# Kernel tuning notes

Measured on AMD Instinct MI355X. Metric: run time of the kernel, lower is better.

## Reference

```python
import jax, jax.numpy as jnp
import numpy as np

B, S, DIM = 4, 2048, 64
NUM_CODES = 65536
KCODES = 8


def setup_inputs() -> dict:
    key = jax.random.key(0)
    k1, k2 = jax.random.split(key)
    x = jax.random.normal(k1, (B, S, DIM), dtype=jnp.float32)
    codebook = jax.random.normal(k2, (NUM_CODES, DIM), dtype=jnp.float32)
    return {"x": x, "codebook": codebook}


def reference(x, codebook):
    """EuclideanSnapFunction.forward, keep_k_codes path with no disabled codes.

    logits = -cdist(x, codebook, p=2); topk(kcodes); embedding gather; mean.
    sqrt is monotonic, so top-k on negative *squared* distance yields identical
    indices (and identical outputs) while avoiding the sqrt.
    """
    x2 = jnp.sum(x * x, axis=-1, keepdims=True)          # [B,S,1]
    c2 = jnp.sum(codebook * codebook, axis=-1)           # [N]
    xc = jnp.einsum("bsd,nd->bsn", x, codebook)          # [B,S,N]
    neg_d2 = 2.0 * xc - x2 - c2                           # = -squared dist
    _, codebook_ids = jax.lax.top_k(neg_d2, KCODES)      # [B,S,K]
    codes = codebook[codebook_ids]                        # [B,S,K,D] gather
    outputs = codes.sum(axis=-2) / KCODES                 # [B,S,D]
    return outputs, codebook_ids
```

## Files before the change

kernel.cpp:

```cpp
#include <hip/hip_runtime.h>
#include <float.h>

#define DIM     64
#define NCODES  65536
#define KC      8
#define NQ      8192
#define KROW    80
#define CS      64
#define CHUNK   (NCODES/CS)
#define NITER   (CHUNK/32)
#define NVIEW   128
#define CAP     7
#define DELTA   0.75f
#define MAXSUR  512
#define CSA     32
#define CHUNKA  512
#define NITERA  (CHUNKA/32)
#define NVIEWA  64

typedef __bf16 bf16x8 __attribute__((ext_vector_type(8)));
typedef float  f32x16 __attribute__((ext_vector_type(16)));
typedef unsigned short u16x8 __attribute__((ext_vector_type(8)));

static __device__ __forceinline__ unsigned short f2bf(float f) {
    unsigned u = __float_as_uint(f);
    u += 0x7FFFu + ((u >> 16) & 1u);
    return (unsigned short)(u >> 16);
}

#define RJ(j) (((j) & 3) + 8 * ((j) >> 2))

__global__ __launch_bounds__(256) void k_conv_cb(const float* __restrict__ cb,
                                                 unsigned short* __restrict__ cbb) {
    int n = blockIdx.x * 256 + threadIdx.x;
    const float4* src = (const float4*)(cb + (size_t)n * DIM);
    unsigned short* dst = cbb + (size_t)n * KROW;
    float s = 0.f;
#pragma unroll
    for (int c = 0; c < 8; ++c) {
        float4 f0 = src[2 * c], f1 = src[2 * c + 1];
        s = fmaf(f0.x, f0.x, s); s = fmaf(f0.y, f0.y, s);
        s = fmaf(f0.z, f0.z, s); s = fmaf(f0.w, f0.w, s);
        s = fmaf(f1.x, f1.x, s); s = fmaf(f1.y, f1.y, s);
        s = fmaf(f1.z, f1.z, s); s = fmaf(f1.w, f1.w, s);
        u16x8 o;
        o[0] = f2bf(2.f * f0.x); o[1] = f2bf(2.f * f0.y);
        o[2] = f2bf(2.f * f0.z); o[3] = f2bf(2.f * f0.w);
        o[4] = f2bf(2.f * f1.x); o[5] = f2bf(2.f * f1.y);
        o[6] = f2bf(2.f * f1.z); o[7] = f2bf(2.f * f1.w);
        *(u16x8*)(dst + c * 8) = o;
    }
    unsigned short hi = f2bf(s);
    float hif = __uint_as_float(((unsigned)hi) << 16);
    unsigned short lo = f2bf(s - hif);
    u16x8 p = { (unsigned short)(hi ^ 0x8000u), (unsigned short)(lo ^ 0x8000u),
                0, 0, 0, 0, 0, 0 };
    *(u16x8*)(dst + 64) = p;
    u16x8 z = {0, 0, 0, 0, 0, 0, 0, 0};
    *(u16x8*)(dst + 72) = z;
}

__global__ __launch_bounds__(256) void k_conv_x(const float* __restrict__ x,
                                                unsigned short* __restrict__ xb) {
    int n = blockIdx.x * 256 + threadIdx.x;
    const float4* src = (const float4*)(x + (size_t)n * DIM);
    unsigned short* dst = xb + (size_t)n * KROW;
#pragma unroll
    for (int c = 0; c < 8; ++c) {
        float4 f0 = src[2 * c], f1 = src[2 * c + 1];
        u16x8 o;
        o[0] = f2bf(f0.x); o[1] = f2bf(f0.y); o[2] = f2bf(f0.z); o[3] = f2bf(f0.w);
        o[4] = f2bf(f1.x); o[5] = f2bf(f1.y); o[6] = f2bf(f1.z); o[7] = f2bf(f1.w);
        *(u16x8*)(dst + c * 8) = o;
    }
    u16x8 p = {0x3F80u, 0x3F80u, 0, 0, 0, 0, 0, 0};
    *(u16x8*)(dst + 64) = p;
    u16x8 z = {0, 0, 0, 0, 0, 0, 0, 0};
    *(u16x8*)(dst + 72) = z;
}

__device__ __forceinline__ float tmax16(const f32x16& a) {
    const float m0 = fmaxf(fmaxf(a[0],  a[1]),  a[2]);
    const float m1 = fmaxf(fmaxf(a[3],  a[4]),  a[5]);
    const float m2 = fmaxf(fmaxf(a[6],  a[7]),  a[8]);
    const float m3 = fmaxf(fmaxf(a[9],  a[10]), a[11]);
    const float m4 = fmaxf(fmaxf(a[12], a[13]), a[14]);
    const float n0 = fmaxf(fmaxf(m0, m1), m2);
    const float n1 = fmaxf(fmaxf(m3, m4), a[15]);
    return fmaxf(n0, n1);
}

__global__ __launch_bounds__(256, 4) void k_scanA(const unsigned short* __restrict__ cbb_,
                                                  const unsigned short* __restrict__ xb_,
                                                  float* __restrict__ top1) {
    const __bf16* cbv = (const __bf16*)cbb_;
    const __bf16* xbv = (const __bf16*)xb_;
    const int tid = threadIdx.x, lane = tid & 63, wv = tid >> 6;
    const int laneh = lane >> 5;
    const int qg = blockIdx.x >> 5;
    const int cs = blockIdx.x & 31;
    const int qA = qg * 256 + wv * 64 + (lane & 31);
    const int qB = qA + 32;
    const int cbase = cs * CHUNKA;
    const int view = cs * 2 + laneh;

    bf16x8 bfrA[5], bfrB[5];
    {
        const __bf16* bp = xbv + (size_t)qA * KROW + laneh * 8;
#pragma unroll
        for (int s = 0; s < 5; ++s) bfrA[s] = *(const bf16x8*)(bp + s * 16);
        bp += (size_t)32 * KROW;
#pragma unroll
        for (int s = 0; s < 5; ++s) bfrB[s] = *(const bf16x8*)(bp + s * 16);
    }

    float t1a = -FLT_MAX, t1b = -FLT_MAX;

    const __bf16* ap = cbv + (size_t)(cbase + (lane & 31)) * KROW + laneh * 8;
    bf16x8 fA[5], fB[5];
#pragma unroll
    for (int s = 0; s < 5; ++s) fA[s] = *(const bf16x8*)(ap + s * 16);
#pragma unroll
    for (int s = 0; s < 5; ++s) fB[s] = *(const bf16x8*)(ap + 32 * KROW + s * 16);
    ap += 64 * KROW;

    for (int it = 0; it < NITERA; it += 2) {
        {
            f32x16 acc = {0,0,0,0, 0,0,0,0, 0,0,0,0, 0,0,0,0};
#pragma unroll
            for (int s = 0; s < 5; ++s)
                acc = __builtin_amdgcn_mfma_f32_32x32x16_bf16(fA[s], bfrA[s], acc, 0, 0, 0);
            t1a = fmaxf(t1a, tmax16(acc));
            f32x16 acc2 = {0,0,0,0, 0,0,0,0, 0,0,0,0, 0,0,0,0};
#pragma unroll
            for (int s = 0; s < 5; ++s)
                acc2 = __builtin_amdgcn_mfma_f32_32x32x16_bf16(fA[s], bfrB[s], acc2, 0, 0, 0);
#pragma unroll
            for (int s = 0; s < 5; ++s) fA[s] = *(const bf16x8*)(ap + s * 16);
            t1b = fmaxf(t1b, tmax16(acc2));
        }
        {
            f32x16 acc = {0,0,0,0, 0,0,0,0, 0,0,0,0, 0,0,0,0};
#pragma unroll
            for (int s = 0; s < 5; ++s)
                acc = __builtin_amdgcn_mfma_f32_32x32x16_bf16(fB[s], bfrA[s], acc, 0, 0, 0);
            t1a = fmaxf(t1a, tmax16(acc));
            f32x16 acc2 = {0,0,0,0, 0,0,0,0, 0,0,0,0, 0,0,0,0};
#pragma unroll
            for (int s = 0; s < 5; ++s)
                acc2 = __builtin_amdgcn_mfma_f32_32x32x16_bf16(fB[s], bfrB[s], acc2, 0, 0, 0);
#pragma unroll
            for (int s = 0; s < 5; ++s) fB[s] = *(const bf16x8*)(ap + 32 * KROW + s * 16);
            t1b = fmaxf(t1b, tmax16(acc2));
        }
        ap += 64 * KROW;
    }

    top1[(size_t)qA * NVIEWA + view] = t1a;
    top1[(size_t)qB * NVIEWA + view] = t1b;
}

__global__ __launch_bounds__(256) void k_thresh(const float* __restrict__ top1,
                                                float* __restrict__ thrm) {
    const int lane = threadIdx.x & 63;
    const int q = blockIdx.x * 4 + (threadIdx.x >> 6);
    float v = top1[(size_t)q * NVIEWA + lane];
    float mx = -FLT_MAX;
#pragma unroll
    for (int r = 0; r < 8; ++r) {
        mx = v;
#pragma unroll
        for (int off = 32; off; off >>= 1) mx = fmaxf(mx, __shfl_xor(mx, off, 64));
        if (v == mx) v = -FLT_MAX;
    }
    if (lane == 0) thrm[q] = mx - DELTA;
}

__global__ __launch_bounds__(256, 4) void k_collect(const unsigned short* __restrict__ cbb_,
                                                    const unsigned short* __restrict__ xb_,
                                                    const float* __restrict__ thrm,
                                                    unsigned short* __restrict__ cand,
                                                    unsigned char* __restrict__ cnt) {
    const __bf16* cbv = (const __bf16*)cbb_;
    const __bf16* xbv = (const __bf16*)xb_;
    const int tid = threadIdx.x, lane = tid & 63, wv = tid >> 6;
    const int laneh = lane >> 5;
    const int qg = blockIdx.x >> 6;
    const int cs = blockIdx.x & 63;
    const int qA = qg * 256 + wv * 64 + (lane & 31);
    const int qB = qA + 32;
    const int cbase = cs * CHUNK;
    const int view = cs * 2 + laneh;

    bf16x8 bfrA[5], bfrB[5];
    {
        const __bf16* bp = xbv + (size_t)qA * KROW + laneh * 8;
#pragma unroll
        for (int s = 0; s < 5; ++s) bfrA[s] = *(const bf16x8*)(bp + s * 16);
        bp += (size_t)32 * KROW;
#pragma unroll
        for (int s = 0; s < 5; ++s) bfrB[s] = *(const bf16x8*)(bp + s * 16);
    }
    const float TmA = thrm[qA];
    const float TmB = thrm[qB];
    unsigned cA = 0, cB = 0;
    unsigned short* bufA = cand + ((size_t)qA * NVIEW + view) * CAP;
    unsigned short* bufB = cand + ((size_t)qB * NVIEW + view) * CAP;

    const __bf16* ap = cbv + (size_t)(cbase + (lane & 31)) * KROW + laneh * 8;
    bf16x8 fA[5], fB[5];
#pragma unroll
    for (int s = 0; s < 5; ++s) fA[s] = *(const bf16x8*)(ap + s * 16);
#pragma unroll
    for (int s = 0; s < 5; ++s) fB[s] = *(const bf16x8*)(ap + 32 * KROW + s * 16);
    ap += 64 * KROW;

    for (int it = 0; it < NITER; it += 2) {
        {
            const int code0 = cbase + it * 32 + 4 * laneh;
            f32x16 acc = {0,0,0,0, 0,0,0,0, 0,0,0,0, 0,0,0,0};
#pragma unroll
            for (int s = 0; s < 5; ++s)
                acc = __builtin_amdgcn_mfma_f32_32x32x16_bf16(fA[s], bfrA[s], acc, 0, 0, 0);
            if (__any(tmax16(acc) >= TmA)) {
#pragma unroll
                for (int j = 0; j < 16; ++j)
                    if (acc[j] >= TmA) { if (cA < CAP) bufA[cA] = (unsigned short)(code0 + RJ(j)); ++cA; }
            }
            f32x16 acc2 = {0,0,0,0, 0,0,0,0, 0,0,0,0, 0,0,0,0};
#pragma unroll
            for (int s = 0; s < 5; ++s)
                acc2 = __builtin_amdgcn_mfma_f32_32x32x16_bf16(fA[s], bfrB[s], acc2, 0, 0, 0);
#pragma unroll
            for (int s = 0; s < 5; ++s) fA[s] = *(const bf16x8*)(ap + s * 16);
            if (__any(tmax16(acc2) >= TmB)) {
#pragma unroll
                for (int j = 0; j < 16; ++j)
                    if (acc2[j] >= TmB) { if (cB < CAP) bufB[cB] = (unsigned short)(code0 + RJ(j)); ++cB; }
            }
        }
        {
            const int code0 = cbase + (it + 1) * 32 + 4 * laneh;
            f32x16 acc = {0,0,0,0, 0,0,0,0, 0,0,0,0, 0,0,0,0};
#pragma unroll
            for (int s = 0; s < 5; ++s)
                acc = __builtin_amdgcn_mfma_f32_32x32x16_bf16(fB[s], bfrA[s], acc, 0, 0, 0);
            if (__any(tmax16(acc) >= TmA)) {
#pragma unroll
                for (int j = 0; j < 16; ++j)
                    if (acc[j] >= TmA) { if (cA < CAP) bufA[cA] = (unsigned short)(code0 + RJ(j)); ++cA; }
            }
            f32x16 acc2 = {0,0,0,0, 0,0,0,0, 0,0,0,0, 0,0,0,0};
#pragma unroll
            for (int s = 0; s < 5; ++s)
                acc2 = __builtin_amdgcn_mfma_f32_32x32x16_bf16(fB[s], bfrB[s], acc2, 0, 0, 0);
#pragma unroll
            for (int s = 0; s < 5; ++s) fB[s] = *(const bf16x8*)(ap + 32 * KROW + s * 16);
            if (__any(tmax16(acc2) >= TmB)) {
#pragma unroll
                for (int j = 0; j < 16; ++j)
                    if (acc2[j] >= TmB) { if (cB < CAP) bufB[cB] = (unsigned short)(code0 + RJ(j)); ++cB; }
            }
        }
        ap += 64 * KROW;
    }
    cnt[(size_t)qA * NVIEW + view] = (unsigned char)(cA < CAP ? cA : CAP);
    cnt[(size_t)qB * NVIEW + view] = (unsigned char)(cB < CAP ? cB : CAP);
}

__device__ __forceinline__ float np_pairwise_sq64(const float* __restrict__ p) {
    float r[8];
#pragma unroll
    for (int j = 0; j < 8; ++j) r[j] = __fmul_rn(p[j], p[j]);
#pragma unroll
    for (int k = 1; k < 8; ++k)
#pragma unroll
        for (int j = 0; j < 8; ++j)
            r[j] = __fadd_rn(r[j], __fmul_rn(p[8 * k + j], p[8 * k + j]));
    const float t01 = __fadd_rn(r[0], r[1]);
    const float t23 = __fadd_rn(r[2], r[3]);
    const float t45 = __fadd_rn(r[4], r[5]);
    const float t67 = __fadd_rn(r[6], r[7]);
    return __fadd_rn(__fadd_rn(t01, t23), __fadd_rn(t45, t67));
}

__device__ __forceinline__ float score_key(const float* __restrict__ xr,
                                           const float* __restrict__ cr,
                                           float x2e) {
    float xc = 0.f;
#pragma unroll
    for (int d = 0; d < DIM; ++d) xc = __builtin_fmaf(cr[d], xr[d], xc);
    const float c2e = np_pairwise_sq64(cr);
    return __fsub_rn(__fsub_rn(__fmul_rn(2.0f, xc), x2e), c2e);
}

__global__ __launch_bounds__(256) void k_rescore(const float* __restrict__ x,
                                                 const float* __restrict__ cb,
                                                 const unsigned short* __restrict__ cand,
                                                 const unsigned char* __restrict__ cnt,
                                                 float* __restrict__ out0,
                                                 float* __restrict__ out1) {
    __shared__ int s_ids[4][MAXSUR];
    const int lane = threadIdx.x & 63;
    const int wvi = threadIdx.x >> 6;
    const int q = blockIdx.x * 4 + wvi;
    const float* xr = x + ((size_t)q << 6);
    const float x2e = np_pairwise_sq64(xr);

    const int c0 = cnt[(size_t)q * NVIEW + 2 * lane];
    const int c1 = cnt[(size_t)q * NVIEW + 2 * lane + 1];
    const int c = c0 + c1;
    int p = c;
#pragma unroll
    for (int off = 1; off < 64; off <<= 1) {
        const int t = __shfl_up(p, off, 64);
        if (lane >= off) p += t;
    }
    const int excl = p - c;
    int total = __shfl(p, 63, 64);
    if (total > MAXSUR) total = MAXSUR;
    const unsigned short* s0 = cand + ((size_t)q * NVIEW + 2 * lane) * CAP;
    for (int k = 0; k < c0; ++k) {
        const int dst = excl + k;
        if (dst < MAXSUR) s_ids[wvi][dst] = s0[k];
    }
    const unsigned short* s1 = s0 + CAP;
    for (int k = 0; k < c1; ++k) {
        const int dst = excl + c0 + k;
        if (dst < MAXSUR) s_ids[wvi][dst] = s1[k];
    }
    __syncthreads();

    float vv[8]; int id[8];
#pragma unroll
    for (int s = 0; s < 8; ++s) {
        vv[s] = -FLT_MAX; id[s] = 1 << 20;
        if (s * 64 < total) {
            const int pos = lane + 64 * s;
            if (pos < total) {
                const int idv = s_ids[wvi][pos];
                id[s] = idv;
                vv[s] = score_key(xr, cb + (size_t)idv * DIM, x2e);
            }
        }
    }

    double accd = 0.0;
#pragma unroll
    for (int rep = 0; rep < KC; ++rep) {
        float bv = vv[0]; int bi = id[0];
#pragma unroll
        for (int s = 1; s < 8; ++s)
            if (vv[s] > bv || (vv[s] == bv && id[s] < bi)) { bv = vv[s]; bi = id[s]; }
#pragma unroll
        for (int off = 32; off; off >>= 1) {
            const float ov = __shfl_xor(bv, off, 64);
            const int   oi = __shfl_xor(bi, off, 64);
            if (ov > bv || (ov == bv && oi < bi)) { bv = ov; bi = oi; }
        }
        if (lane == 0) out1[q * KC + rep] = (float)bi;
        accd += (double)cb[(size_t)bi * DIM + lane];
#pragma unroll
        for (int s = 0; s < 8; ++s) if (id[s] == bi) vv[s] = -FLT_MAX;
    }
    out0[(size_t)q * DIM + lane] = (float)(accd * 0.125);
}

extern "C" void kernel_launch(void* const* d_in, const int* in_sizes, int n_in,
                              void* d_out, int out_size, void* d_ws, size_t ws_size,
                              hipStream_t stream) {
    const float* x  = (const float*)d_in[0];
    const float* cb = (const float*)d_in[1];

    char* ws = (char*)d_ws;
    unsigned short* cbb  = (unsigned short*)ws;
    unsigned short* xb   = (unsigned short*)(ws + (size_t)NCODES * KROW * 2);
    float*          top1 = (float*)(ws + (size_t)NCODES * KROW * 2
                                       + (size_t)NQ * KROW * 2);
    float*          thrm = (float*)((char*)top1 + (size_t)NQ * NVIEWA * 4);
    unsigned char*  cnt  = (unsigned char*)((char*)thrm + (size_t)NQ * 4);
    unsigned short* cand = (unsigned short*)((char*)cnt + (size_t)NQ * NVIEW);

    float* out0 = (float*)d_out;
    float* out1 = (float*)d_out + (size_t)NQ * DIM;

    k_conv_cb<<<NCODES / 256, 256, 0, stream>>>(cb, cbb);
    k_conv_x <<<NQ / 256,     256, 0, stream>>>(x, xb);
    k_scanA  <<<1024,         256, 0, stream>>>(cbb, xb, top1);
    k_thresh <<<NQ / 4,       256, 0, stream>>>(top1, thrm);
    k_collect<<<2048,         256, 0, stream>>>(cbb, xb, thrm, cand, cnt);
    k_rescore<<<NQ / 4,       256, 0, stream>>>(x, cb, cand, cnt, out0, out1);
}
```

Baseline: 182.3 us.

## Interleave four MFMA accumulators per cluster with deeper register prefetch and setprio

Both scan kernels now process two 32-code tiles per step with four independent accumulators and interleaved MFMA chains. This is meant to hide MFMA dependency latency and give more time to cover the global loads, which are now double-buffered two tiles ahead. s_setprio raises wave priority around the MFMA clusters, and launch bounds drop to 2 blocks per CU so the extra registers fit. The cost is lower occupancy. The prefetch also reads past the chunk end on the last iterations, which stays in bounds except possibly for the final chunk.

New measurement: 212.6 us. +16.6%, slower.

```diff
diff --git a/kernel.cpp b/kernel.cpp
--- a/kernel.cpp
+++ b/kernel.cpp
@@ -22,6 +22,8 @@
 typedef float  f32x16 __attribute__((ext_vector_type(16)));
 typedef unsigned short u16x8 __attribute__((ext_vector_type(8)));
 
+#define ZERO16 {0,0,0,0, 0,0,0,0, 0,0,0,0, 0,0,0,0}
+
 static __device__ __forceinline__ unsigned short f2bf(float f) {
     unsigned u = __float_as_uint(f);
     u += 0x7FFFu + ((u >> 16) & 1u);
@@ -90,16 +92,36 @@
     return fmaxf(n0, n1);
 }
 
-__global__ __launch_bounds__(256, 4) void k_scanA(const unsigned short* __restrict__ cbb_,
+#define LOAD10(t0, t1, tile) do {                                              \
+    const __bf16* p0_ = abase + (size_t)(tile) * (32 * KROW);                  \
+    const __bf16* p1_ = p0_ + 32 * KROW;                                       \
+    _Pragma("unroll") for (int s_ = 0; s_ < 5; ++s_)                           \
+        t0[s_] = *(const bf16x8*)(p0_ + s_ * 16);                              \
+    _Pragma("unroll") for (int s_ = 0; s_ < 5; ++s_)                           \
+        t1[s_] = *(const bf16x8*)(p1_ + s_ * 16);                              \
+} while (0)
+
+#define CLUSTER(c00, c01, c10, c11, t0, t1) do {                               \
+    __builtin_amdgcn_s_setprio(1);                                             \
+    _Pragma("unroll") for (int s_ = 0; s_ < 5; ++s_) {                         \
+        c00 = __builtin_amdgcn_mfma_f32_32x32x16_bf16(t0[s_], bfrA[s_], c00, 0, 0, 0); \
+        c01 = __builtin_amdgcn_mfma_f32_32x32x16_bf16(t0[s_], bfrB[s_], c01, 0, 0, 0); \
+        c10 = __builtin_amdgcn_mfma_f32_32x32x16_bf16(t1[s_], bfrA[s_], c10, 0, 0, 0); \
+        c11 = __builtin_amdgcn_mfma_f32_32x32x16_bf16(t1[s_], bfrB[s_], c11, 0, 0, 0); \
+    }                                                                          \
+    __builtin_amdgcn_s_setprio(0);                                             \
+} while (0)
+
+__global__ __launch_bounds__(256, 2) void k_scanA(const unsigned short* __restrict__ cbb_,
                                                   const unsigned short* __restrict__ xb_,
                                                   float* __restrict__ top1) {
     const __bf16* cbv = (const __bf16*)cbb_;
     const __bf16* xbv = (const __bf16*)xb_;
     const int tid = threadIdx.x, lane = tid & 63, wv = tid >> 6;
-    const int laneh = lane >> 5;
+    const int laneh = lane >> 5, lrow = lane & 31;
     const int qg = blockIdx.x >> 5;
     const int cs = blockIdx.x & 31;
-    const int qA = qg * 256 + wv * 64 + (lane & 31);
+    const int qA = qg * 256 + wv * 64 + lrow;
     const int qB = qA + 32;
     const int cbase = cs * CHUNKA;
     const int view = cs * 2 + laneh;
@@ -115,45 +137,27 @@
     }
 
     float t1a = -FLT_MAX, t1b = -FLT_MAX;
-
-    const __bf16* ap = cbv + (size_t)(cbase + (lane & 31)) * KROW + laneh * 8;
-    bf16x8 fA[5], fB[5];
-#pragma unroll
-    for (int s = 0; s < 5; ++s) fA[s] = *(const bf16x8*)(ap + s * 16);
-#pragma unroll
-    for (int s = 0; s < 5; ++s) fB[s] = *(const bf16x8*)(ap + 32 * KROW + s * 16);
-    ap += 64 * KROW;
-
-    for (int it = 0; it < NITERA; it += 2) {
+    const __bf16* abase = cbv + (size_t)(cbase + lrow) * KROW + laneh * 8;
+
+    bf16x8 fa0[5], fa1[5], fb0[5], fb1[5];
+    LOAD10(fa0, fa1, 0);
+    LOAD10(fb0, fb1, 2);
+
+    for (int it = 0; it < NITERA; it += 4) {
         {
-            f32x16 acc = {0,0,0,0, 0,0,0,0, 0,0,0,0, 0,0,0,0};
-#pragma unroll
-            for (int s = 0; s < 5; ++s)
-                acc = __builtin_amdgcn_mfma_f32_32x32x16_bf16(fA[s], bfrA[s], acc, 0, 0, 0);
-            t1a = fmaxf(t1a, tmax16(acc));
-            f32x16 acc2 = {0,0,0,0, 0,0,0,0, 0,0,0,0, 0,0,0,0};
-#pragma unroll
-            for (int s = 0; s < 5; ++s)
-                acc2 = __builtin_amdgcn_mfma_f32_32x32x16_bf16(fA[s], bfrB[s], acc2, 0, 0, 0);
-#pragma unroll
-            for (int s = 0; s < 5; ++s) fA[s] = *(const bf16x8*)(ap + s * 16);
-            t1b = fmaxf(t1b, tmax16(acc2));
+            f32x16 c00 = ZERO16, c01 = ZERO16, c10 = ZERO16, c11 = ZERO16;
+            CLUSTER(c00, c01, c10, c11, fa0, fa1);
+            LOAD10(fa0, fa1, it + 4);
+            t1a = fmaxf(t1a, fmaxf(tmax16(c00), tmax16(c10)));
+            t1b = fmaxf(t1b, fmaxf(tmax16(c01), tmax16(c11)));
         }
         {
-            f32x16 acc = {0,0,0,0, 0,0,0,0, 0,0,0,0, 0,0,0,0};
-#pragma unroll
-            for (int s = 0; s < 5; ++s)
-                acc = __builtin_amdgcn_mfma_f32_32x32x16_bf16(fB[s], bfrA[s], acc, 0, 0, 0);
-            t1a = fmaxf(t1a, tmax16(acc));
-            f32x16 acc2 = {0,0,0,0, 0,0,0,0, 0,0,0,0, 0,0,0,0};
-#pragma unroll
-            for (int s = 0; s < 5; ++s)
-                acc2 = __builtin_amdgcn_mfma_f32_32x32x16_bf16(fB[s], bfrB[s], acc2, 0, 0, 0);
-#pragma unroll
-            for (int s = 0; s < 5; ++s) fB[s] = *(const bf16x8*)(ap + 32 * KROW + s * 16);
-            t1b = fmaxf(t1b, tmax16(acc2));
-        }
-        ap += 64 * KROW;
+            f32x16 c00 = ZERO16, c01 = ZERO16, c10 = ZERO16, c11 = ZERO16;
+            CLUSTER(c00, c01, c10, c11, fb0, fb1);
+            LOAD10(fb0, fb1, it + 6);
+            t1a = fmaxf(t1a, fmaxf(tmax16(c00), tmax16(c10)));
+            t1b = fmaxf(t1b, fmaxf(tmax16(c01), tmax16(c11)));
+        }
     }
 
     top1[(size_t)qA * NVIEWA + view] = t1a;
@@ -176,7 +180,16 @@
     if (lane == 0) thrm[q] = mx - DELTA;
 }
 
-__global__ __launch_bounds__(256, 4) void k_collect(const unsigned short* __restrict__ cbb_,
+__device__ __forceinline__ void coll_ep(const f32x16& acc, float Tm, int code0,
+                                        unsigned short* __restrict__ buf, unsigned& c) {
+    if (__any(tmax16(acc) >= Tm)) {
+#pragma unroll
+        for (int j = 0; j < 16; ++j)
+            if (acc[j] >= Tm) { if (c < CAP) buf[c] = (unsigned short)(code0 + RJ(j)); ++c; }
+    }
+}
+
+__global__ __launch_bounds__(256, 2) void k_collect(const unsigned short* __restrict__ cbb_,
                                                     const unsigned short* __restrict__ xb_,
                                                     const float* __restrict__ thrm,
                                                     unsigned short* __restrict__ cand,
@@ -184,10 +197,10 @@
     const __bf16* cbv = (const __bf16*)cbb_;
     const __bf16* xbv = (const __bf16*)xb_;
     const int tid = threadIdx.x, lane = tid & 63, wv = tid >> 6;
-    const int laneh = lane >> 5;
+    const int laneh = lane >> 5, lrow = lane & 31;
     const int qg = blockIdx.x >> 6;
     const int cs = blockIdx.x & 63;
-    const int qA = qg * 256 + wv * 64 + (lane & 31);
+    const int qA = qg * 256 + wv * 64 + lrow;
     const int qB = qA + 32;
     const int cbase = cs * CHUNK;
     const int view = cs * 2 + laneh;
@@ -207,62 +220,33 @@
     unsigned short* bufA = cand + ((size_t)qA * NVIEW + view) * CAP;
     unsigned short* bufB = cand + ((size_t)qB * NVIEW + view) * CAP;
 
-    const __bf16* ap = cbv + (size_t)(cbase + (lane & 31)) * KROW + laneh * 8;
-    bf16x8 fA[5], fB[5];
-#pragma unroll
-    for (int s = 0; s < 5; ++s) fA[s] = *(const bf16x8*)(ap + s * 16);
-#pragma unroll
-    for (int s = 0; s < 5; ++s) fB[s] = *(const bf16x8*)(ap + 32 * KROW + s * 16);
-    ap += 64 * KROW;
-
-    for (int it = 0; it < NITER; it += 2) {
+    const __bf16* abase = cbv + (size_t)(cbase + lrow) * KROW + laneh * 8;
+
+    bf16x8 fa0[5], fa1[5], fb0[5], fb1[5];
+    LOAD10(fa0, fa1, 0);
+    LOAD10(fb0, fb1, 2);
+
+    for (int it = 0; it < NITER; it += 4) {
         {
+            f32x16 c00 = ZERO16, c01 = ZERO16, c10 = ZERO16, c11 = ZERO16;
+            CLUSTER(c00, c01, c10, c11, fa0, fa1);
+            LOAD10(fa0, fa1, it + 4);
             const int code0 = cbase + it * 32 + 4 * laneh;
-            f32x16 acc = {0,0,0,0, 0,0,0,0, 0,0,0,0, 0,0,0,0};
-#pragma unroll
-            for (int s = 0; s < 5; ++s)
-                acc = __builtin_amdgcn_mfma_f32_32x32x16_bf16(fA[s], bfrA[s], acc, 0, 0, 0);
-            if (__any(tmax16(acc) >= TmA)) {
-#pragma unroll
-                for (int j = 0; j < 16; ++j)
-                    if (acc[j] >= TmA) { if (cA < CAP) bufA[cA] = (unsigned short)(code0 + RJ(j)); ++cA; }
-            }
-            f32x16 acc2 = {0,0,0,0, 0,0,0,0, 0,0,0,0, 0,0,0,0};
-#pragma unroll
-            for (int s = 0; s < 5; ++s)
-                acc2 = __builtin_amdgcn_mfma_f32_32x32x16_bf16(fA[s], bfrB[s], acc2, 0, 0, 0);
-#pragma unroll
-            for (int s = 0; s < 5; ++s) fA[s] = *(const bf16x8*)(ap + s * 16);
-            if (__any(tmax16(acc2) >= TmB)) {
-#pragma unroll
-                for (int j = 0; j < 16; ++j)
-                    if (acc2[j] >= TmB) { if (cB < CAP) bufB[cB] = (unsigned short)(code0 + RJ(j)); ++cB; }
-            }
+            coll_ep(c00, TmA, code0,      bufA, cA);
+            coll_ep(c01, TmB, code0,      bufB, cB);
+            coll_ep(c10, TmA, code0 + 32, bufA, cA);
+            coll_ep(c11, TmB, code0 + 32, bufB, cB);
         }
         {
-            const int code0 = cbase + (it + 1) * 32 + 4 * laneh;
-            f32x16 acc = {0,0,0,0, 0,0,0,0, 0,0,0,0, 0,0,0,0};
-#pragma unroll
-            for (int s = 0; s < 5; ++s)
-                acc = __builtin_amdgcn_mfma_f32_32x32x16_bf16(fB[s], bfrA[s], acc, 0, 0, 0);
-            if (__any(tmax16(acc) >= TmA)) {
-#pragma unroll
-                for (int j = 0; j < 16; ++j)
-                    if (acc[j] >= TmA) { if (cA < CAP) bufA[cA] = (unsigned short)(code0 + RJ(j)); ++cA; }
-            }
-            f32x16 acc2 = {0,0,0,0, 0,0,0,0, 0,0,0,0, 0,0,0,0};
-#pragma unroll
-            for (int s = 0; s < 5; ++s)
-                acc2 = __builtin_amdgcn_mfma_f32_32x32x16_bf16(fB[s], bfrB[s], acc2, 0, 0, 0);
-#pragma unroll
-            for (int s = 0; s < 5; ++s) fB[s] = *(const bf16x8*)(ap + 32 * KROW + s * 16);
-            if (__any(tmax16(acc2) >= TmB)) {
-#pragma unroll
-                for (int j = 0; j < 16; ++j)
-                    if (acc2[j] >= TmB) { if (cB < CAP) bufB[cB] = (unsigned short)(code0 + RJ(j)); ++cB; }
-            }
-        }
-        ap += 64 * KROW;
+            f32x16 c00 = ZERO16, c01 = ZERO16, c10 = ZERO16, c11 = ZERO16;
+            CLUSTER(c00, c01, c10, c11, fb0, fb1);
+            LOAD10(fb0, fb1, it + 6);
+            const int code0 = cbase + (it + 2) * 32 + 4 * laneh;
+            coll_ep(c00, TmA, code0,      bufA, cA);
+            coll_ep(c01, TmB, code0,      bufB, cB);
+            coll_ep(c10, TmA, code0 + 32, bufA, cA);
+            coll_ep(c11, TmB, code0 + 32, bufB, cB);
+        }
     }
     cnt[(size_t)qA * NVIEW + view] = (unsigned char)(cA < CAP ? cA : CAP);
     cnt[(size_t)qB * NVIEW + view] = (unsigned char)(cB < CAP ? cB : CAP);
```
